# Kernel tuning notes

Measured on AMD Instinct MI355X. Metric: run time of the kernel, lower is better.

Reference implementation:

```python
import jax, jax.numpy as jnp
import numpy as np

IN_DIMS = (8, 8, 8, 8)
OUT_DIMS = (8, 8, 8, 8)
RANKS = (1, 16, 16, 16, 1)
BATCH = 4096


def setup_inputs() -> dict:
    key = jax.random.key(0)
    ks = jax.random.split(key, 6)
    n_in = int(np.prod(IN_DIMS))
    n_out = int(np.prod(OUT_DIMS))
    d = len(IN_DIMS)
    # t3f glorot: total matrix variance 2/(n_in+n_out), split evenly across cores/ranks
    lamb = 2.0 / (n_in + n_out)
    cv = (lamb / np.prod(RANKS)) ** (1.0 / d)
    core_std = float(np.sqrt(cv))
    cores = {}
    for i in range(d):
        shp = (RANKS[i], IN_DIMS[i], OUT_DIMS[i], RANKS[i + 1])
        cores[f"core{i}"] = core_std * jax.random.normal(ks[i], shp, dtype=jnp.float32)
    x = jax.random.normal(ks[4], (BATCH, n_in), dtype=jnp.float32)
    b = 0.1 * jnp.ones((n_out,), dtype=jnp.float32)
    return {"x": x, **cores, "b": b}


def tt_dense(x, cores):
    """y = x @ M, M the TT-matrix with cores [r_{k-1}, a_k, b_k, r_k]."""
    B = x.shape[0]
    rest = int(np.prod(IN_DIMS[1:]))
    # t: [B, P(out dims done), r, a_k, rest(in dims todo)]
    t = x.reshape(B, 1, 1, IN_DIMS[0], rest)
    for k, core in enumerate(cores):
        # contract rank r and input mode a_k -> produce output mode b_k and next rank q
        t = jnp.einsum('zpras,rabq->zpbqs', t, core)
        z, p, bd, q, s = t.shape
        if k < len(cores) - 1:
            a_next = IN_DIMS[k + 1]
            t = t.reshape(z, p * bd, q, a_next, s // a_next)
        else:
            t = t.reshape(z, p * bd)  # q == s == 1
    return t  # [B, prod(OUT_DIMS)]


def reference(x, core0, core1, core2, core3, b):
    y = tt_dense(x, [core0, core1, core2, core3])
    return jax.nn.relu(y + b)
```

## Files before the change

### kernel.cpp

```cpp
#include <hip/hip_runtime.h>
#include <hip/hip_bf16.h>
#include <cstdint>
#include <cstddef>


#define GM 4096
#define GN 4096
#define GK 4096
#define NT (GK / 64)

typedef __attribute__((ext_vector_type(8))) short short8_t;
typedef __attribute__((ext_vector_type(4))) float float4_t;

__device__ __forceinline__ unsigned short f2bf(float f) {
  union { float f; uint32_t u; } v; v.f = f;
  uint32_t u = v.u;
  uint32_t r = (u + 0x7fffu + ((u >> 16) & 1u)) >> 16;
  return (unsigned short)r;
}

__global__ __launch_bounds__(256) void prep_kernel(
    const float* __restrict__ c0, const float* __restrict__ c1,
    const float* __restrict__ c2, const float* __restrict__ c3,
    float* __restrict__ G01, float* __restrict__ G23t) {
  int idx = blockIdx.x * 256 + threadIdx.x;
  if (idx < 65536) {
    int r2 = idx & 15;
    int b01 = (idx >> 4) & 63;
    int a01 = idx >> 10;
    int a0 = a01 >> 3, a1 = a01 & 7, b0 = b01 >> 3, b1 = b01 & 7;
    float s = 0.f;
#pragma unroll
    for (int r1 = 0; r1 < 16; ++r1)
      s += c0[(a0 * 8 + b0) * 16 + r1] * c1[((r1 * 8 + a1) * 8 + b1) * 16 + r2];
    G01[idx] = s;
  } else {
    int t = idx - 65536;
    int a23 = t & 63;
    int b23 = (t >> 6) & 63;
    int r2 = t >> 12;
    int a2 = a23 >> 3, a3 = a23 & 7, b2 = b23 >> 3, b3 = b23 & 7;
    float s = 0.f;
#pragma unroll
    for (int r3 = 0; r3 < 16; ++r3)
      s += c2[((r2 * 8 + a2) * 8 + b2) * 16 + r3] * c3[(r3 * 8 + a3) * 8 + b3];
    G23t[t] = s;
  }
}

__global__ __launch_bounds__(256) void mt_convert(
    const float* __restrict__ G01, const float* __restrict__ G23t,
    unsigned short* __restrict__ Mt,
    const float* __restrict__ x, unsigned short* __restrict__ xb) {
  int bid = blockIdx.x;
  int tid = threadIdx.x;
  if (bid < 1024) {
    int a01 = bid >> 4;
    int g = bid & 15;

    float acc[4][16];
#pragma unroll
    for (int j = 0; j < 4; ++j)
#pragma unroll
      for (int i = 0; i < 16; ++i) acc[j][i] = 0.f;

    for (int r2 = 0; r2 < 16; ++r2) {
      float gv[4];
#pragma unroll
      for (int j = 0; j < 4; ++j)
        gv[j] = G01[(a01 * 64 + g * 4 + j) * 16 + r2];
      const float* src = G23t + r2 * 4096 + tid * 16;
      float4_t v0 = *(const float4_t*)(src);
      float4_t v1 = *(const float4_t*)(src + 4);
      float4_t v2 = *(const float4_t*)(src + 8);
      float4_t v3 = *(const float4_t*)(src + 12);
#pragma unroll
      for (int j = 0; j < 4; ++j) {
#pragma unroll
        for (int l = 0; l < 4; ++l) {
          acc[j][l]      += gv[j] * v0[l];
          acc[j][4 + l]  += gv[j] * v1[l];
          acc[j][8 + l]  += gv[j] * v2[l];
          acc[j][12 + l] += gv[j] * v3[l];
        }
      }
    }

    int b23 = tid >> 2;
    int a23base = (tid & 3) * 16;
#pragma unroll
    for (int j = 0; j < 4; ++j) {
      short8_t o0, o1;
#pragma unroll
      for (int i = 0; i < 8; ++i) {
        o0[i] = (short)f2bf(acc[j][i]);
        o1[i] = (short)f2bf(acc[j][8 + i]);
      }
      size_t base = (size_t)((g * 4 + j) * 64 + b23) * GK + a01 * 64 + a23base;
      *(short8_t*)(Mt + base) = o0;
      *(short8_t*)(Mt + base + 8) = o1;
    }
  } else {
    int i = ((bid - 1024) * 256 + tid) * 8;
    float4_t a = *(const float4_t*)(x + i);
    float4_t b = *(const float4_t*)(x + i + 4);
    short8_t o;
    o[0] = (short)f2bf(a[0]); o[1] = (short)f2bf(a[1]);
    o[2] = (short)f2bf(a[2]); o[3] = (short)f2bf(a[3]);
    o[4] = (short)f2bf(b[0]); o[5] = (short)f2bf(b[1]);
    o[6] = (short)f2bf(b[2]); o[7] = (short)f2bf(b[3]);
    *(short8_t*)(xb + i) = o;
  }
}

__global__ __launch_bounds__(512, 2) void gemm_bias_relu(
    const unsigned short* __restrict__ A, const unsigned short* __restrict__ Bt,
    const float* __restrict__ bias, float* __restrict__ C) {
  extern __shared__ __align__(16) unsigned short lds[];

  const int tid = threadIdx.x;
  const int bswz = blockIdx.x;
  const int xcd = bswz & 7, li = bswz >> 3;
  const int row0 = ((xcd >> 1) * 4 + (li >> 3)) * 256;
  const int col0 = ((xcd & 1) * 8 + (li & 7)) * 256;
  const int wave = tid >> 6, lane = tid & 63;
  const int wm = wave >> 2, wn = wave & 3;
  const int half = lane >> 4, mrow = lane & 15;

  const int r0 = tid >> 3, p0 = tid & 7, h0 = (p0 - r0) & 7;
  const unsigned short* Abase = A + (size_t)(row0 + r0) * GK + h0 * 8;
  const unsigned short* Bbase = Bt + (size_t)(col0 + r0) * GK + h0 * 8;
  const int dA = r0 * 64 + p0 * 8;
  const int dB = dA + 16384;

#define GLD(SRC, DST)                                                  \
  __builtin_amdgcn_global_load_lds(                                    \
      (const __attribute__((address_space(1))) void*)(SRC),            \
      (__attribute__((address_space(3))) void*)(lds + (DST)), 16, 0, 0)
#define STAGE_A(G, KT, BUF)                                            \
  do {                                                                 \
    const unsigned short* s_ = Abase + (size_t)(G) * 128 * GK + (KT) * 64; \
    GLD(s_, (BUF) * 32768 + (G) * 8192 + dA);                          \
    GLD(s_ + (size_t)64 * GK, (BUF) * 32768 + (G) * 8192 + dA + 4096); \
  } while (0)
#define STAGE_B(G, KT, BUF)                                            \
  do {                                                                 \
    const unsigned short* s_ = Bbase + (size_t)(G) * 128 * GK + (KT) * 64; \
    GLD(s_, (BUF) * 32768 + (G) * 8192 + dB);                          \
    GLD(s_ + (size_t)64 * GK, (BUF) * 32768 + (G) * 8192 + dB + 4096); \
  } while (0)

  const int arow = wm * 128 + mrow;
  const int aoff0 = arow * 64 + ((half + arow) & 7) * 8;
  const int aoff1 = aoff0 ^ 32;
  const int brow = wn * 64 + mrow;
  const int boff0 = 16384 + brow * 64 + ((half + brow) & 7) * 8;
  const int boff1 = boff0 ^ 32;

#define RD_A(DST, BUF, Q)                                                   \
  do {                                                                      \
    _Pragma("unroll")                                                       \
    for (int ii = 0; ii < 2; ++ii) {                                        \
      DST[ii * 2 + 0] =                                                     \
          *(const short8_t*)&lds[(BUF)*32768 + aoff0 + (2*(Q)+ii) * 1024];  \
      DST[ii * 2 + 1] =                                                     \
          *(const short8_t*)&lds[(BUF)*32768 + aoff1 + (2*(Q)+ii) * 1024];  \
    }                                                                       \
  } while (0)
#define RD_B(DST, BUF)                                                      \
  do {                                                                      \
    _Pragma("unroll")                                                       \
    for (int n = 0; n < 4; ++n) {                                           \
      DST[n * 2 + 0] =                                                      \
          *(const short8_t*)&lds[(BUF)*32768 + boff0 + n * 1024];           \
      DST[n * 2 + 1] =                                                      \
          *(const short8_t*)&lds[(BUF)*32768 + boff1 + n * 1024];           \
    }                                                                       \
  } while (0)
#define MFMA_Q(Q, AF, BV)                                                   \
  do {                                                                      \
    __builtin_amdgcn_s_setprio(1);                                          \
    _Pragma("unroll")                                                       \
    for (int ks = 0; ks < 2; ++ks)                                          \
      _Pragma("unroll")                                                     \
      for (int ii = 0; ii < 2; ++ii)                                        \
        _Pragma("unroll")                                                   \
        for (int n = 0; n < 4; ++n)                                         \
          acc[2*(Q)+ii][n] = __builtin_amdgcn_mfma_f32_16x16x32_bf16(       \
              AF[ii * 2 + ks], BV[n * 2 + ks], acc[2*(Q)+ii][n], 0, 0, 0);  \
    __builtin_amdgcn_s_setprio(0);                                          \
  } while (0)
#define BAR()                                                               \
  do {                                                                      \
    __builtin_amdgcn_s_barrier();                                           \
    __builtin_amdgcn_sched_barrier(0);                                      \
  } while (0)

  float4_t acc[8][4];
#pragma unroll
  for (int i = 0; i < 8; ++i)
#pragma unroll
    for (int n = 0; n < 4; ++n) acc[i][n] = (float4_t){0.f, 0.f, 0.f, 0.f};

  short8_t b0v[8], b1v[8], afE[4], afO[4];

  STAGE_A(0, 0, 0); STAGE_A(1, 0, 0); STAGE_B(0, 0, 0); STAGE_B(1, 0, 0);
  STAGE_B(0, 1, 1); STAGE_B(1, 1, 1);
  asm volatile("s_waitcnt vmcnt(4)" ::: "memory");
  BAR();
  RD_B(b0v, 0);
  RD_A(afE, 0, 0);

  for (int kt = 0; kt < NT; kt += 2) {
    RD_A(afO, 0, 1);
    STAGE_A(0, kt + 1, 1);
    MFMA_Q(0, afE, b0v);
    BAR();
    RD_A(afE, 0, 2);
    STAGE_A(1, kt + 1, 1);
    if (kt + 2 < NT) STAGE_B(0, kt + 2, 0);
    MFMA_Q(1, afO, b0v);
    BAR();
    RD_A(afO, 0, 3);
    if (kt + 2 < NT) STAGE_B(1, kt + 2, 0);
    MFMA_Q(2, afE, b0v);
    if (kt + 2 < NT)
      asm volatile("s_waitcnt vmcnt(4)" ::: "memory");
    else
      asm volatile("s_waitcnt vmcnt(0)" ::: "memory");
    BAR();
    RD_B(b1v, 1);
    RD_A(afE, 1, 0);
    MFMA_Q(3, afO, b0v);
    BAR();

    RD_A(afO, 1, 1);
    if (kt + 2 < NT) STAGE_A(0, kt + 2, 0);
    MFMA_Q(0, afE, b1v);
    BAR();
    RD_A(afE, 1, 2);
    if (kt + 2 < NT) STAGE_A(1, kt + 2, 0);
    if (kt + 3 < NT) STAGE_B(0, kt + 3, 1);
    MFMA_Q(1, afO, b1v);
    BAR();
    RD_A(afO, 1, 3);
    if (kt + 3 < NT) STAGE_B(1, kt + 3, 1);
    MFMA_Q(2, afE, b1v);
    if (kt + 3 < NT)
      asm volatile("s_waitcnt vmcnt(4)" ::: "memory");
    else
      asm volatile("s_waitcnt vmcnt(0)" ::: "memory");
    BAR();
    if (kt + 2 < NT) { RD_B(b0v, 0); RD_A(afE, 0, 0); }
    MFMA_Q(3, afO, b1v);
    BAR();
  }

#undef BAR
#undef MFMA_Q
#undef RD_B
#undef RD_A
#undef STAGE_B
#undef STAGE_A
#undef GLD

#pragma unroll
  for (int n = 0; n < 4; ++n) {
    int col = col0 + wn * 64 + n * 16 + mrow;
    float bcol = bias[col];
#pragma unroll
    for (int i = 0; i < 8; ++i) {
#pragma unroll
      for (int r = 0; r < 4; ++r) {
        int row = row0 + wm * 128 + i * 16 + half * 4 + r;
        float v = acc[i][n][r] + bcol;
        C[(size_t)row * GN + col] = v > 0.f ? v : 0.f;
      }
    }
  }
}

extern "C" void kernel_launch(void* const* d_in, const int* in_sizes, int n_in,
                              void* d_out, int out_size, void* d_ws, size_t ws_size,
                              hipStream_t stream) {
  const float* x  = (const float*)d_in[0];
  const float* c0 = (const float*)d_in[1];
  const float* c1 = (const float*)d_in[2];
  const float* c2 = (const float*)d_in[3];
  const float* c3 = (const float*)d_in[4];
  const float* b  = (const float*)d_in[5];
  float* out = (float*)d_out;

  unsigned short* xb = (unsigned short*)d_ws;
  unsigned short* Mt = (unsigned short*)((char*)d_ws + (32u << 20));
  float* G01 = (float*)((char*)d_ws + (64u << 20));
  float* G23t = G01 + 65536;

  static bool lds_configured = false;
  if (!lds_configured) {
    (void)hipFuncSetAttribute((const void*)gemm_bias_relu,
                              hipFuncAttributeMaxDynamicSharedMemorySize,
                              131072);
    lds_configured = true;
  }

  prep_kernel<<<512, 256, 0, stream>>>(c0, c1, c2, c3, G01, G23t);
  mt_convert<<<1024 + (GM * GK) / (256 * 8), 256, 0, stream>>>(
      G01, G23t, Mt, x, xb);
  gemm_bias_relu<<<(GM / 256) * (GN / 256), 512, 131072, stream>>>(
      xb, Mt, b, out);
}
```

Measured before the change: 252.9 us.

## Restructure GEMM main loop into quadrant tiles with reordered LDS staging

Replaces the eight-phase per-k-tile schedule, which held full B fragments and row-quarter A fragments, with a four-quadrant TILE schedule. Each quadrant uses half-A by half-B fragments, so register fragments are reused across two MFMA blocks. Global-to-LDS staging and the vmcnt waits are reordered, and the prologue now preloads A for the next tile. This trades a different LDS read pattern, more barriers and explicit lgkmcnt waits for lower fragment register pressure and a changed copy/compute overlap.

Measured after the change: 256.5 us. Within noise of the previous version (+1.4%).

```diff
diff --git a/kernel.cpp b/kernel.cpp
--- a/kernel.cpp
+++ b/kernel.cpp
@@ -157,41 +157,71 @@
   const int boff0 = 16384 + brow * 64 + ((half + brow) & 7) * 8;
   const int boff1 = boff0 ^ 32;
 
-#define RD_A(DST, BUF, Q)                                                   \
+#define RD_AH(DST, BUF, MT0)                                                \
   do {                                                                      \
     _Pragma("unroll")                                                       \
-    for (int ii = 0; ii < 2; ++ii) {                                        \
-      DST[ii * 2 + 0] =                                                     \
-          *(const short8_t*)&lds[(BUF)*32768 + aoff0 + (2*(Q)+ii) * 1024];  \
-      DST[ii * 2 + 1] =                                                     \
-          *(const short8_t*)&lds[(BUF)*32768 + aoff1 + (2*(Q)+ii) * 1024];  \
+    for (int m = 0; m < 4; ++m) {                                           \
+      DST[m * 2 + 0] =                                                      \
+          *(const short8_t*)&lds[(BUF)*32768 + aoff0 + ((MT0) + m) * 1024]; \
+      DST[m * 2 + 1] =                                                      \
+          *(const short8_t*)&lds[(BUF)*32768 + aoff1 + ((MT0) + m) * 1024]; \
     }                                                                       \
   } while (0)
-#define RD_B(DST, BUF)                                                      \
+#define RD_BH(DST, BUF, NT0)                                                \
   do {                                                                      \
     _Pragma("unroll")                                                       \
-    for (int n = 0; n < 4; ++n) {                                           \
+    for (int n = 0; n < 2; ++n) {                                           \
       DST[n * 2 + 0] =                                                      \
-          *(const short8_t*)&lds[(BUF)*32768 + boff0 + n * 1024];           \
+          *(const short8_t*)&lds[(BUF)*32768 + boff0 + ((NT0) + n) * 1024]; \
       DST[n * 2 + 1] =                                                      \
-          *(const short8_t*)&lds[(BUF)*32768 + boff1 + n * 1024];           \
+          *(const short8_t*)&lds[(BUF)*32768 + boff1 + ((NT0) + n) * 1024]; \
     }                                                                       \
   } while (0)
-#define MFMA_Q(Q, AF, BV)                                                   \
+#define MFMA_H(MB, AF, NB, BF)                                              \
   do {                                                                      \
     __builtin_amdgcn_s_setprio(1);                                          \
     _Pragma("unroll")                                                       \
     for (int ks = 0; ks < 2; ++ks)                                          \
       _Pragma("unroll")                                                     \
-      for (int ii = 0; ii < 2; ++ii)                                        \
+      for (int m = 0; m < 4; ++m)                                           \
         _Pragma("unroll")                                                   \
-        for (int n = 0; n < 4; ++n)                                         \
-          acc[2*(Q)+ii][n] = __builtin_amdgcn_mfma_f32_16x16x32_bf16(       \
-              AF[ii * 2 + ks], BV[n * 2 + ks], acc[2*(Q)+ii][n], 0, 0, 0);  \
+        for (int n = 0; n < 2; ++n)                                         \
+          acc[(MB) + m][(NB) + n] = __builtin_amdgcn_mfma_f32_16x16x32_bf16(\
+              AF[m * 2 + ks], BF[n * 2 + ks], acc[(MB) + m][(NB) + n],      \
+              0, 0, 0);                                                     \
     __builtin_amdgcn_s_setprio(0);                                          \
   } while (0)
-#define BAR()                                                               \
+
+#define TILE(CB, OB, KT)                                                    \
   do {                                                                      \
+                                                 \
+    RD_AH(a0f, CB, 0);                                                      \
+    RD_BH(b0f, CB, 0);                                                      \
+    if ((KT) + 1 < NT) STAGE_B(1, (KT) + 1, OB);                            \
+    __builtin_amdgcn_s_barrier();                                           \
+    asm volatile("s_waitcnt lgkmcnt(0)" ::: "memory");                      \
+    MFMA_H(0, a0f, 0, b0f);                                                 \
+    __builtin_amdgcn_s_barrier();                                           \
+                                                 \
+    RD_BH(b1f, CB, 2);                                                      \
+    __builtin_amdgcn_s_barrier();                                           \
+    asm volatile("s_waitcnt lgkmcnt(0)" ::: "memory");                      \
+    MFMA_H(0, a0f, 2, b1f);                                                 \
+    __builtin_amdgcn_s_barrier();                                           \
+                                                 \
+    RD_AH(a1f, CB, 4);                                                      \
+    if ((KT) + 2 < NT) STAGE_B(0, (KT) + 2, CB);                            \
+    __builtin_amdgcn_s_barrier();                                           \
+    asm volatile("s_waitcnt lgkmcnt(0)" ::: "memory");                      \
+    MFMA_H(4, a1f, 2, b1f);                                                 \
+    __builtin_amdgcn_s_barrier();                                           \
+          \
+    if ((KT) + 2 < NT) { STAGE_A(0, (KT) + 2, CB); STAGE_A(1, (KT) + 2, CB); } \
+    MFMA_H(4, a1f, 0, b0f);                                                 \
+    if ((KT) + 2 < NT)                                                      \
+      asm volatile("s_waitcnt vmcnt(6)" ::: "memory");                      \
+    else if ((KT) + 1 < NT)                                                 \
+      asm volatile("s_waitcnt vmcnt(0)" ::: "memory");                      \
     __builtin_amdgcn_s_barrier();                                           \
     __builtin_amdgcn_sched_barrier(0);                                      \
   } while (0)
@@ -202,64 +232,23 @@
 #pragma unroll
     for (int n = 0; n < 4; ++n) acc[i][n] = (float4_t){0.f, 0.f, 0.f, 0.f};
 
-  short8_t b0v[8], b1v[8], afE[4], afO[4];
+  short8_t a0f[8], a1f[8], b0f[4], b1f[4];
 
   STAGE_A(0, 0, 0); STAGE_A(1, 0, 0); STAGE_B(0, 0, 0); STAGE_B(1, 0, 0);
-  STAGE_B(0, 1, 1); STAGE_B(1, 1, 1);
-  asm volatile("s_waitcnt vmcnt(4)" ::: "memory");
-  BAR();
-  RD_B(b0v, 0);
-  RD_A(afE, 0, 0);
+  STAGE_B(0, 1, 1); STAGE_A(0, 1, 1); STAGE_A(1, 1, 1);
+  asm volatile("s_waitcnt vmcnt(6)" ::: "memory");
+  __builtin_amdgcn_s_barrier();
+  __builtin_amdgcn_sched_barrier(0);
 
   for (int kt = 0; kt < NT; kt += 2) {
-    RD_A(afO, 0, 1);
-    STAGE_A(0, kt + 1, 1);
-    MFMA_Q(0, afE, b0v);
-    BAR();
-    RD_A(afE, 0, 2);
-    STAGE_A(1, kt + 1, 1);
-    if (kt + 2 < NT) STAGE_B(0, kt + 2, 0);
-    MFMA_Q(1, afO, b0v);
-    BAR();
-    RD_A(afO, 0, 3);
-    if (kt + 2 < NT) STAGE_B(1, kt + 2, 0);
-    MFMA_Q(2, afE, b0v);
-    if (kt + 2 < NT)
-      asm volatile("s_waitcnt vmcnt(4)" ::: "memory");
-    else
-      asm volatile("s_waitcnt vmcnt(0)" ::: "memory");
-    BAR();
-    RD_B(b1v, 1);
-    RD_A(afE, 1, 0);
-    MFMA_Q(3, afO, b0v);
-    BAR();
-
-    RD_A(afO, 1, 1);
-    if (kt + 2 < NT) STAGE_A(0, kt + 2, 0);
-    MFMA_Q(0, afE, b1v);
-    BAR();
-    RD_A(afE, 1, 2);
-    if (kt + 2 < NT) STAGE_A(1, kt + 2, 0);
-    if (kt + 3 < NT) STAGE_B(0, kt + 3, 1);
-    MFMA_Q(1, afO, b1v);
-    BAR();
-    RD_A(afO, 1, 3);
-    if (kt + 3 < NT) STAGE_B(1, kt + 3, 1);
-    MFMA_Q(2, afE, b1v);
-    if (kt + 3 < NT)
-      asm volatile("s_waitcnt vmcnt(4)" ::: "memory");
-    else
-      asm volatile("s_waitcnt vmcnt(0)" ::: "memory");
-    BAR();
-    if (kt + 2 < NT) { RD_B(b0v, 0); RD_A(afE, 0, 0); }
-    MFMA_Q(3, afO, b1v);
-    BAR();
-  }
-
-#undef BAR
-#undef MFMA_Q
-#undef RD_B
-#undef RD_A
+    TILE(0, 1, kt);
+    TILE(1, 0, kt + 1);
+  }
+
+#undef TILE
+#undef MFMA_H
+#undef RD_BH
+#undef RD_AH
 #undef STAGE_B
 #undef STAGE_A
 #undef GLD
```
